# Kernel tuning notes

Hardware: AMD Instinct MI355X
Metric: run time of the kernel (lower is better)

The kernel has to match this reference:

```python
import jax, jax.numpy as jnp
import numpy as np

B, N, E, D = 32, 512, 2048, 128
N_STEPS = 3


def setup_inputs() -> dict:
    key = jax.random.key(0)
    ks = jax.random.split(key, 16)
    s = 0.05
    return {
        "prop_state": jax.random.normal(ks[0], (B, N, D), jnp.float32),
        "edge_states": jax.random.normal(ks[1], (B, E, D), jnp.float32),
        "A": jax.random.uniform(ks[2], (B, N, E), jnp.float32) / E,
        "tem_features": jax.random.normal(ks[3], (B, 64), jnp.float32),
        "link_W": jax.random.normal(ks[4], (D, D), jnp.float32) * s,
        "link_b": jnp.zeros((D,), jnp.float32),
        "reset_W": jax.random.normal(ks[5], (2 * D, D), jnp.float32) * s,
        "reset_b": jnp.zeros((D,), jnp.float32),
        "update_W": jax.random.normal(ks[6], (2 * D, D), jnp.float32) * s,
        "update_b": jnp.zeros((D,), jnp.float32),
        "trans_W": jax.random.normal(ks[7], (2 * D, D), jnp.float32) * s,
        "trans_b": jnp.zeros((D,), jnp.float32),
        "att_W1": jax.random.normal(ks[8], (D, D), jnp.float32) * s,
        "att_b1": jnp.zeros((D,), jnp.float32),
        "att_W2": jax.random.normal(ks[9], (D, 1), jnp.float32) * s,
        "att_b2": jnp.zeros((1,), jnp.float32),
        "out_W": jax.random.normal(ks[10], (D, D), jnp.float32) * s,
        "out_b": jnp.zeros((D,), jnp.float32),
    }


def reference(prop_state, edge_states, A, tem_features,
              link_W, link_b, reset_W, reset_b, update_W, update_b,
              trans_W, trans_b, att_W1, att_b1, att_W2, att_b2, out_W, out_b):
    init_node = prop_state
    init_edge = edge_states
    for _ in range(N_STEPS):
        edge_states = edge_states @ link_W + link_b              # [B,E,D]
        a_cur = jnp.einsum('bne,bed->bnd', A, edge_states)       # [B,N,D]
        a = jnp.concatenate([a_cur, prop_state], axis=2)         # [B,N,2D]
        r = jax.nn.sigmoid(a @ reset_W + reset_b)
        z = jax.nn.sigmoid(a @ update_W + update_b)
        joined = jnp.concatenate([a_cur, r * prop_state], axis=2)
        h_hat = jnp.tanh(joined @ trans_W + trans_b)
        prop_state = (1.0 - z) * prop_state + z * h_hat
    # attention pooling
    atten = jnp.tanh(prop_state @ att_W1 + att_b1) @ att_W2 + att_b2   # [B,N,1]
    Aw = jax.nn.softmax(jnp.transpose(atten, (0, 2, 1)), axis=2)       # [B,1,N]
    out = jnp.tanh(prop_state @ out_W + out_b)                         # [B,N,D]
    mul = jnp.einsum('bqn,bnd->bqd', Aw, out)                          # [B,1,D]
    graph_out = jnp.tanh(jnp.squeeze(mul, axis=1))                     # [B,D]
    # residual block: mean over concatenated node+edge initial states
    feat = jnp.concatenate([init_node, init_edge], axis=1)             # [B,N+E,D]
    residual = jnp.mean(feat, axis=1)                                  # [B,D]
    res = jax.nn.relu(graph_out + residual)
    return res, mul, edge_states
```

## Files before the change

### kernel.cpp

```cpp
#include <hip/hip_runtime.h>
#include <hip/hip_bf16.h>


typedef unsigned short u16;
typedef __attribute__((ext_vector_type(4))) float f32x4;
typedef __attribute__((ext_vector_type(8))) short bf16x8;

#define DI static __device__ __forceinline__

DI u16 f2bf(float f) {
    unsigned u = __builtin_bit_cast(unsigned, f);
    return (u16)((u + 0x7fffu + ((u >> 16) & 1u)) >> 16);
}
DI float bf2f(u16 h) { return __builtin_bit_cast(float, ((unsigned)h) << 16); }

DI bf16x8 cvt8(float4 a, float4 b) {
    u16 tmp[8] = {f2bf(a.x), f2bf(a.y), f2bf(a.z), f2bf(a.w),
                  f2bf(b.x), f2bf(b.y), f2bf(b.z), f2bf(b.w)};
    return *(const bf16x8*)tmp;
}

DI int imgIdx(int k, int n) {
    return (((k >> 5) * 128 + n) * 4 + (((k >> 3) & 3) ^ ((n >> 1) & 3))) * 8 + (k & 7);
}
DI bf16x8 wfragG(const u16* __restrict__ img, int kc, int tt, int l15, int quad) {
    return *(const bf16x8*)&img[(((kc * 128 + tt * 16 + l15) * 4) + (quad ^ ((l15 >> 1) & 3))) * 8];
}

#define MFMA16(a, b, c) __builtin_amdgcn_mfma_f32_16x16x32_bf16(a, b, c, 0, 0, 0)

__global__ __launch_bounds__(256) void k_prep1(
    const float* __restrict__ linkW, const float* __restrict__ resetW,
    const float* __restrict__ updateW, const float* __restrict__ transW,
    const float* __restrict__ attW1, const float* __restrict__ outW,
    float* __restrict__ W2, u16* __restrict__ linkImg, u16* __restrict__ WrImg,
    u16* __restrict__ WzImg, u16* __restrict__ WhImg, u16* __restrict__ attW1Img,
    u16* __restrict__ outWImg)
{
    int blk = blockIdx.x, t = threadIdx.x;
    if (blk < 64) {
        int idx = blk * 256 + t;
        int r = idx >> 7, c = idx & 127;
        float acc = 0.f;
        for (int k = 0; k < 128; k++) acc += linkW[r * 128 + k] * linkW[k * 128 + c];
        W2[r * 128 + c] = acc;
    } else {
        const float* src; u16* dst; int base;
        if (blk < 68)      { src = resetW;  dst = WrImg;    base = 64; }
        else if (blk < 72) { src = updateW; dst = WzImg;    base = 68; }
        else if (blk < 76) { src = transW;  dst = WhImg;    base = 72; }
        else if (blk < 78) { src = linkW;   dst = linkImg;  base = 76; }
        else if (blk < 80) { src = attW1;   dst = attW1Img; base = 78; }
        else               { src = outW;    dst = outWImg;  base = 80; }
        int off = (blk - base) * 8192;
        for (int i = 0; i < 32; i++) {
            int e = off + t + i * 256;
            int k = e >> 7, n = e & 127;
            dst[imgIdx(k, n)] = f2bf(src[e]);
        }
    }
}

__global__ __launch_bounds__(256) void k_prep2(
    const float* __restrict__ linkW, const float* __restrict__ linkb,
    const float* __restrict__ W2, u16* __restrict__ W3Img, float* __restrict__ ebias)
{
    int blk = blockIdx.x, t = threadIdx.x;
    if (blk < 64) {
        int idx = blk * 256 + t;
        int r = idx >> 7, c = idx & 127;
        float acc = 0.f;
        for (int k = 0; k < 128; k++) acc += W2[r * 128 + k] * linkW[k * 128 + c];
        W3Img[imgIdx(r, c)] = f2bf(acc);
    } else if (t < 128) {
        float acc = linkb[t];
        for (int k = 0; k < 128; k++) acc += linkb[k] * (W2[k * 128 + t] + linkW[k * 128 + t]);
        ebias[t] = acc;
    }
}

__global__ __launch_bounds__(256) void k_te(
    const float* __restrict__ E0, u16* __restrict__ Eswz, float* __restrict__ resid)
{
    __shared__ alignas(16) u16 sT[4096];
    __shared__ float sCol[128];
    int t = threadIdx.x, kc = blockIdx.x, b = blockIdx.y;
    const float* Eb = E0 + (size_t)b * 262144 + (size_t)kc * 32 * 128;
    if (t < 128) sCol[t] = 0.f;
    float part[4] = {0.f, 0.f, 0.f, 0.f};
    int ncol = (t & 31) * 4;
    for (int i = 0; i < 4; i++) {
        int f4i = t + i * 256;
        int k5 = f4i >> 5;
        float4 v = *(const float4*)&Eb[k5 * 128 + ncol];
        int g = k5 >> 3, o = k5 & 7;
        float vv[4] = {v.x, v.y, v.z, v.w};
#pragma unroll
        for (int j = 0; j < 4; j++) {
            int n = ncol + j;
            sT[(n * 4 + (g ^ ((n >> 1) & 3))) * 8 + o] = f2bf(vv[j]);
            part[j] += vv[j];
        }
    }
    __syncthreads();
#pragma unroll
    for (int j = 0; j < 4; j++) atomicAdd(&sCol[ncol + j], part[j]);
    u16* dst = Eswz + (size_t)b * 262144 + (size_t)kc * 4096;
    ((uint4*)dst)[t] = ((const uint4*)sT)[t];
    ((uint4*)dst)[t + 256] = ((const uint4*)sT)[t + 256];
    __syncthreads();
    if (t < 128) atomicAdd(&resid[b * 128 + t], sCol[t]);
}

__global__ __launch_bounds__(256, 3) void k_g0(
    const float* __restrict__ A, const u16* __restrict__ Eswz,
    u16* __restrict__ aOut, float* __restrict__ rowsum)
{
    __shared__ float sAcc[4][16][128];
    __shared__ float sRs[4][16];
    int t = threadIdx.x, wid = t >> 6, lane = t & 63, l15 = lane & 15, quad = lane >> 4;
    int bx = blockIdx.x;
    int g = bx >> 8, rmod = bx & 255;
    int b = (rmod & 7) + 8 * g;
    int s = (rmod >> 3) & 31;
    size_t r0 = (size_t)b * 512 + (size_t)s * 16;
    const u16* Eb = Eswz + (size_t)b * 262144;
    const float* Ar = A + (r0 + l15) * 2048;
    int kbase = wid * 16;

    f32x4 acc[8];
#pragma unroll
    for (int i = 0; i < 8; i++) acc[i] = (f32x4){0.f, 0.f, 0.f, 0.f};
    float rsum = 0.f;

    float4 xc = *(const float4*)&Ar[kbase * 32 + quad * 8];
    float4 yc = *(const float4*)&Ar[kbase * 32 + quad * 8 + 4];
    bf16x8 bc[8];
#pragma unroll
    for (int tt = 0; tt < 8; tt++) bc[tt] = wfragG(Eb, kbase, tt, l15, quad);

    for (int kc = 0; kc < 16; kc++) {
        int kg = kbase + kc;
        float4 xn, yn; bf16x8 bn[8];
        if (kc < 15) {
            xn = *(const float4*)&Ar[(kg + 1) * 32 + quad * 8];
            yn = *(const float4*)&Ar[(kg + 1) * 32 + quad * 8 + 4];
#pragma unroll
            for (int tt = 0; tt < 8; tt++) bn[tt] = wfragG(Eb, kg + 1, tt, l15, quad);
        }
        rsum += xc.x + xc.y + xc.z + xc.w + yc.x + yc.y + yc.z + yc.w;
        bf16x8 af = cvt8(xc, yc);
#pragma unroll
        for (int tt = 0; tt < 8; tt++) acc[tt] = MFMA16(af, bc[tt], acc[tt]);
        if (kc < 15) {
            xc = xn; yc = yn;
#pragma unroll
            for (int tt = 0; tt < 8; tt++) bc[tt] = bn[tt];
        }
    }
    rsum += __shfl_xor(rsum, 16);
    rsum += __shfl_xor(rsum, 32);
    if (quad == 0) sRs[wid][l15] = rsum;
#pragma unroll
    for (int tt = 0; tt < 8; tt++)
#pragma unroll
        for (int r = 0; r < 4; r++)
            sAcc[wid][quad * 4 + r][tt * 16 + l15] = acc[tt][r];
    __syncthreads();
    {
        int row = t >> 4, c8 = (t & 15) * 8;
        u16 o[8];
#pragma unroll
        for (int j = 0; j < 8; j++) {
            float v = sAcc[0][row][c8 + j] + sAcc[1][row][c8 + j] +
                      sAcc[2][row][c8 + j] + sAcc[3][row][c8 + j];
            o[j] = f2bf(v);
        }
        *(uint4*)&aOut[(r0 + row) * 128 + c8] = *(const uint4*)o;
    }
    if (t < 16)
        rowsum[r0 + t] = sRs[0][t] + sRs[1][t] + sRs[2][t] + sRs[3][t];
}

__global__ __launch_bounds__(64) void k_gates(
    u16* __restrict__ aBuf, const float* __restrict__ pIn, float* __restrict__ pOut,
    const float* __restrict__ rowsum,
    const u16* __restrict__ linkImg, const u16* __restrict__ WrImg,
    const u16* __restrict__ WzImg, const u16* __restrict__ WhImg,
    const float* __restrict__ link_b, const float* __restrict__ reset_b,
    const float* __restrict__ update_b, const float* __restrict__ trans_b)
{
    __shared__ alignas(16) u16 sT[16 * 136];
    int t = threadIdx.x, l15 = t & 15, quad = t >> 4;
    size_t r0 = (size_t)blockIdx.x * 16;

    bf16x8 aF[4], pF[4];
#pragma unroll
    for (int kc = 0; kc < 4; kc++) {
        aF[kc] = *(const bf16x8*)&aBuf[(r0 + l15) * 128 + kc * 32 + quad * 8];
        float4 x = *(const float4*)&pIn[(r0 + l15) * 128 + kc * 32 + quad * 8];
        float4 y = *(const float4*)&pIn[(r0 + l15) * 128 + kc * 32 + quad * 8 + 4];
        pF[kc] = cvt8(x, y);
    }

    f32x4 zero4 = {0.f, 0.f, 0.f, 0.f};
    f32x4 acc[8];
#pragma unroll
    for (int i = 0; i < 8; i++) acc[i] = zero4;
#pragma unroll
    for (int kc = 0; kc < 4; kc++)
#pragma unroll
        for (int tt = 0; tt < 8; tt++)
            acc[tt] = MFMA16(aF[kc], wfragG(linkImg, kc, tt, l15, quad), acc[tt]);
    float sv[4];
#pragma unroll
    for (int r = 0; r < 4; r++) sv[r] = rowsum[r0 + quad * 4 + r];
#pragma unroll
    for (int tt = 0; tt < 8; tt++) {
        int col = tt * 16 + l15; float lb = link_b[col];
#pragma unroll
        for (int r = 0; r < 4; r++)
            sT[(quad * 4 + r) * 136 + col] = f2bf(acc[tt][r] + sv[r] * lb);
    }
    __syncthreads();
#pragma unroll
    for (int kc = 0; kc < 4; kc++)
        aF[kc] = *(const bf16x8*)&sT[l15 * 136 + kc * 32 + quad * 8];
#pragma unroll
    for (int i = 0; i < 4; i++) {
        int idx = t + i * 64; int row = idx >> 4, col = (idx & 15) * 8;
        *(uint4*)&aBuf[(r0 + row) * 128 + col] = *(const uint4*)&sT[row * 136 + col];
    }

    f32x4 aR[8], aZ[8];
#pragma unroll
    for (int i = 0; i < 8; i++) { aR[i] = zero4; aZ[i] = zero4; }
#pragma unroll
    for (int kc = 0; kc < 8; kc++) {
        bf16x8 af = (kc < 4) ? aF[kc] : pF[kc - 4];
#pragma unroll
        for (int tt = 0; tt < 8; tt++) {
            aR[tt] = MFMA16(af, wfragG(WrImg, kc, tt, l15, quad), aR[tt]);
            aZ[tt] = MFMA16(af, wfragG(WzImg, kc, tt, l15, quad), aZ[tt]);
        }
    }
    __syncthreads();
#pragma unroll
    for (int tt = 0; tt < 8; tt++) {
        int col = tt * 16 + l15; float rb = reset_b[col], ub = update_b[col];
#pragma unroll
        for (int r = 0; r < 4; r++) {
            float rv = 1.f / (1.f + __expf(-(aR[tt][r] + rb)));
            aZ[tt][r] = 1.f / (1.f + __expf(-(aZ[tt][r] + ub)));
            float p = pIn[(r0 + quad * 4 + r) * 128 + col];
            sT[(quad * 4 + r) * 136 + col] = f2bf(rv * p);
        }
    }
    __syncthreads();
    bf16x8 rpF[4];
#pragma unroll
    for (int kc = 0; kc < 4; kc++)
        rpF[kc] = *(const bf16x8*)&sT[l15 * 136 + kc * 32 + quad * 8];

#pragma unroll
    for (int i = 0; i < 8; i++) aR[i] = zero4;
#pragma unroll
    for (int kc = 0; kc < 8; kc++) {
        bf16x8 af = (kc < 4) ? aF[kc] : rpF[kc - 4];
#pragma unroll
        for (int tt = 0; tt < 8; tt++)
            aR[tt] = MFMA16(af, wfragG(WhImg, kc, tt, l15, quad), aR[tt]);
    }
#pragma unroll
    for (int tt = 0; tt < 8; tt++) {
        int col = tt * 16 + l15; float tb = trans_b[col];
#pragma unroll
        for (int r = 0; r < 4; r++) {
            size_t row = r0 + quad * 4 + r;
            float h = tanhf(aR[tt][r] + tb);
            float z = aZ[tt][r];
            float p = pIn[row * 128 + col];
            pOut[row * 128 + col] = (1.f - z) * p + z * h;
        }
    }
}

__global__ __launch_bounds__(64) void k_att(
    const float* __restrict__ pIn, const u16* __restrict__ attW1Img,
    const u16* __restrict__ outWImg, const float* __restrict__ att_b1,
    const float* __restrict__ att_W2, const float* __restrict__ att_b2,
    const float* __restrict__ out_b, float* __restrict__ atten, float* __restrict__ outPool)
{
    int t = threadIdx.x, l15 = t & 15, quad = t >> 4;
    size_t r0 = (size_t)blockIdx.x * 16;
    bf16x8 pF[4];
#pragma unroll
    for (int kc = 0; kc < 4; kc++) {
        float4 x = *(const float4*)&pIn[(r0 + l15) * 128 + kc * 32 + quad * 8];
        float4 y = *(const float4*)&pIn[(r0 + l15) * 128 + kc * 32 + quad * 8 + 4];
        pF[kc] = cvt8(x, y);
    }
    f32x4 zero4 = {0.f, 0.f, 0.f, 0.f};
    f32x4 aA[8], aO[8];
#pragma unroll
    for (int i = 0; i < 8; i++) { aA[i] = zero4; aO[i] = zero4; }
#pragma unroll
    for (int kc = 0; kc < 4; kc++)
#pragma unroll
        for (int tt = 0; tt < 8; tt++) {
            aA[tt] = MFMA16(pF[kc], wfragG(attW1Img, kc, tt, l15, quad), aA[tt]);
            aO[tt] = MFMA16(pF[kc], wfragG(outWImg, kc, tt, l15, quad), aO[tt]);
        }
    float part[4] = {0.f, 0.f, 0.f, 0.f};
#pragma unroll
    for (int tt = 0; tt < 8; tt++) {
        int col = tt * 16 + l15;
        float b1 = att_b1[col], w2 = att_W2[col], ob = out_b[col];
#pragma unroll
        for (int r = 0; r < 4; r++) {
            part[r] += tanhf(aA[tt][r] + b1) * w2;
            outPool[(r0 + quad * 4 + r) * 128 + col] = tanhf(aO[tt][r] + ob);
        }
    }
    float b2 = att_b2[0];
#pragma unroll
    for (int r = 0; r < 4; r++) {
        float loc = part[r];
        loc += __shfl_xor(loc, 1); loc += __shfl_xor(loc, 2);
        loc += __shfl_xor(loc, 4); loc += __shfl_xor(loc, 8);
        if (l15 == 0) atten[r0 + quad * 4 + r] = loc + b2;
    }
}

__global__ __launch_bounds__(64) void k_eout(
    const float* __restrict__ E0, const u16* __restrict__ W3Img,
    const float* __restrict__ ebias, float* __restrict__ Eout)
{
    int t = threadIdx.x, l15 = t & 15, quad = t >> 4;
    size_t r0 = (size_t)blockIdx.x * 16;
    bf16x8 eF[4];
#pragma unroll
    for (int kc = 0; kc < 4; kc++) {
        float4 x = *(const float4*)&E0[(r0 + l15) * 128 + kc * 32 + quad * 8];
        float4 y = *(const float4*)&E0[(r0 + l15) * 128 + kc * 32 + quad * 8 + 4];
        eF[kc] = cvt8(x, y);
    }
    f32x4 zero4 = {0.f, 0.f, 0.f, 0.f};
    f32x4 acc[8];
#pragma unroll
    for (int i = 0; i < 8; i++) acc[i] = zero4;
#pragma unroll
    for (int kc = 0; kc < 4; kc++)
#pragma unroll
        for (int tt = 0; tt < 8; tt++)
            acc[tt] = MFMA16(eF[kc], wfragG(W3Img, kc, tt, l15, quad), acc[tt]);
#pragma unroll
    for (int tt = 0; tt < 8; tt++) {
        int col = tt * 16 + l15; float eb = ebias[col];
#pragma unroll
        for (int r = 0; r < 4; r++)
            Eout[(r0 + quad * 4 + r) * 128 + col] = acc[tt][r] + eb;
    }
}

__global__ __launch_bounds__(256) void k_fin(
    const float* __restrict__ atten, const float* __restrict__ outPool,
    const float* __restrict__ prop0, const float* __restrict__ resid,
    float* __restrict__ outRes, float* __restrict__ outMul)
{
    __shared__ float swv[512];
    __shared__ float sred[256];
    int t = threadIdx.x, b = blockIdx.x;
    float a0 = atten[b * 512 + t], a1 = atten[b * 512 + 256 + t];
    sred[t] = fmaxf(a0, a1); __syncthreads();
    for (int s = 128; s > 0; s >>= 1) { if (t < s) sred[t] = fmaxf(sred[t], sred[t + s]); __syncthreads(); }
    float mx = sred[0]; __syncthreads();
    float e0 = __expf(a0 - mx), e1 = __expf(a1 - mx);
    swv[t] = e0; swv[t + 256] = e1;
    sred[t] = e0 + e1; __syncthreads();
    for (int s = 128; s > 0; s >>= 1) { if (t < s) sred[t] += sred[t + s]; __syncthreads(); }
    float Z = sred[0]; __syncthreads();
    int col = t & 127, half = t >> 7;
    const float* op = outPool + ((size_t)b * 512 + half * 256) * 128 + col;
    const float* pp = prop0 + ((size_t)b * 512 + half * 256) * 128 + col;
    float accM = 0.f, accN = 0.f;
    for (int n = 0; n < 256; n++) {
        accM += swv[half * 256 + n] * op[(size_t)n * 128];
        accN += pp[(size_t)n * 128];
    }
    sred[t] = accM; __syncthreads();
    float mulv = 0.f;
    if (t < 128) mulv = (sred[t] + sred[t + 128]) / Z;
    __syncthreads();
    sred[t] = accN; __syncthreads();
    if (t < 128) {
        float nodesum = sred[t] + sred[t + 128];
        float rv = (nodesum + resid[b * 128 + t]) * (1.f / 2560.f);
        outMul[b * 128 + t] = mulv;
        outRes[b * 128 + t] = fmaxf(0.f, tanhf(mulv) + rv);
    }
}

extern "C" void kernel_launch(void* const* d_in, const int* in_sizes, int n_in,
                              void* d_out, int out_size, void* d_ws, size_t ws_size,
                              hipStream_t stream)
{
    const float* prop0  = (const float*)d_in[0];
    const float* edge0  = (const float*)d_in[1];
    const float* Amat   = (const float*)d_in[2];
    const float* linkW  = (const float*)d_in[4];
    const float* linkb  = (const float*)d_in[5];
    const float* resetW = (const float*)d_in[6];
    const float* resetb = (const float*)d_in[7];
    const float* updateW= (const float*)d_in[8];
    const float* updateb= (const float*)d_in[9];
    const float* transW = (const float*)d_in[10];
    const float* transb = (const float*)d_in[11];
    const float* attW1  = (const float*)d_in[12];
    const float* attb1  = (const float*)d_in[13];
    const float* attW2  = (const float*)d_in[14];
    const float* attb2  = (const float*)d_in[15];
    const float* outW   = (const float*)d_in[16];
    const float* outb   = (const float*)d_in[17];

    char* w = (char*)d_ws;
    u16*   ws_a_bf    = (u16*)(w);
    float* ws_prop    = (float*)(w + 4194304);
    float* ws_rowsum  = (float*)(w + 12582912);
    float* ws_atten   = (float*)(w + 12648448);
    float* ws_resid   = (float*)(w + 12713984);
    float* ws_W2      = (float*)(w + 12730368);
    float* ws_ebias   = (float*)(w + 12795904);
    u16*   ws_linkImg = (u16*)(w + 12796416);
    u16*   ws_W3Img   = (u16*)(w + 12829184);
    u16*   ws_WrImg   = (u16*)(w + 12861952);
    u16*   ws_WzImg   = (u16*)(w + 12927488);
    u16*   ws_WhImg   = (u16*)(w + 12993024);
    u16*   ws_attW1Img= (u16*)(w + 13058560);
    u16*   ws_outWImg = (u16*)(w + 13091328);

    float* out_res  = (float*)d_out;
    float* out_mul  = out_res + 4096;
    float* out_edge = out_res + 8192;
    u16*   Eswz     = (u16*)out_edge;
    float* outPool  = out_edge + 4194304;

    hipMemsetAsync(ws_resid, 0, 32 * 128 * sizeof(float), stream);
    k_prep1<<<82, 256, 0, stream>>>(linkW, resetW, updateW, transW, attW1, outW,
                                    ws_W2, ws_linkImg, ws_WrImg, ws_WzImg, ws_WhImg,
                                    ws_attW1Img, ws_outWImg);
    k_prep2<<<65, 256, 0, stream>>>(linkW, linkb, ws_W2, ws_W3Img, ws_ebias);
    k_te<<<dim3(64, 32), 256, 0, stream>>>(edge0, Eswz, ws_resid);
    k_g0<<<1024, 256, 0, stream>>>(Amat, Eswz, ws_a_bf, ws_rowsum);
    k_gates<<<1024, 64, 0, stream>>>(ws_a_bf, prop0, ws_prop, ws_rowsum,
                                     ws_linkImg, ws_WrImg, ws_WzImg, ws_WhImg,
                                     linkb, resetb, updateb, transb);
    k_gates<<<1024, 64, 0, stream>>>(ws_a_bf, ws_prop, ws_prop, ws_rowsum,
                                     ws_linkImg, ws_WrImg, ws_WzImg, ws_WhImg,
                                     linkb, resetb, updateb, transb);
    k_gates<<<1024, 64, 0, stream>>>(ws_a_bf, ws_prop, ws_prop, ws_rowsum,
                                     ws_linkImg, ws_WrImg, ws_WzImg, ws_WhImg,
                                     linkb, resetb, updateb, transb);
    k_att<<<1024, 64, 0, stream>>>(ws_prop, ws_attW1Img, ws_outWImg, attb1, attW2, attb2,
                                   outb, ws_atten, outPool);
    k_fin<<<32, 256, 0, stream>>>(ws_atten, outPool, prop0, ws_resid, out_res, out_mul);
    k_eout<<<4096, 64, 0, stream>>>(edge0, ws_W3Img, ws_ebias, out_edge);
}
```

Measured before the change: 396.3 us.

## Fuse attention into last gate step, prefetch weight fragments, parallelize prep and fin

The attention/output projection is folded into the third gate kernel, so the final propagation state no longer makes a round trip through global memory. The gate steps also store a bf16 copy of the state so the next step skips fp32 loads and conversion. Weight fragments are double-buffered in registers across k-chunks to hide load latency, and some __syncthreads are removed. The prep matmuls are split four ways with shuffle reductions, and k_fin uses 512 threads. The removed barriers sit on a shared sT buffer that different lanes read and write, which could be a race risk, and the prefetch buffers raise register pressure.

Measured after the change: 394.2 us. Within noise of the previous version (-0.5%).

```diff
diff --git a/kernel.cpp b/kernel.cpp
--- a/kernel.cpp
+++ b/kernel.cpp
@@ -38,20 +38,25 @@
     u16* __restrict__ outWImg)
 {
     int blk = blockIdx.x, t = threadIdx.x;
-    if (blk < 64) {
+    if (blk < 256) {
         int idx = blk * 256 + t;
-        int r = idx >> 7, c = idx & 127;
+        int out = idx >> 2, q = idx & 3;
+        int r = out >> 7, c = out & 127;
+        const float* ar = linkW + r * 128 + q * 32;
         float acc = 0.f;
-        for (int k = 0; k < 128; k++) acc += linkW[r * 128 + k] * linkW[k * 128 + c];
-        W2[r * 128 + c] = acc;
+#pragma unroll
+        for (int k = 0; k < 32; k++) acc += ar[k] * linkW[(q * 32 + k) * 128 + c];
+        acc += __shfl_xor(acc, 1);
+        acc += __shfl_xor(acc, 2);
+        if (q == 0) W2[out] = acc;
     } else {
         const float* src; u16* dst; int base;
-        if (blk < 68)      { src = resetW;  dst = WrImg;    base = 64; }
-        else if (blk < 72) { src = updateW; dst = WzImg;    base = 68; }
-        else if (blk < 76) { src = transW;  dst = WhImg;    base = 72; }
-        else if (blk < 78) { src = linkW;   dst = linkImg;  base = 76; }
-        else if (blk < 80) { src = attW1;   dst = attW1Img; base = 78; }
-        else               { src = outW;    dst = outWImg;  base = 80; }
+        if (blk < 260)      { src = resetW;  dst = WrImg;    base = 256; }
+        else if (blk < 264) { src = updateW; dst = WzImg;    base = 260; }
+        else if (blk < 268) { src = transW;  dst = WhImg;    base = 264; }
+        else if (blk < 270) { src = linkW;   dst = linkImg;  base = 268; }
+        else if (blk < 272) { src = attW1;   dst = attW1Img; base = 270; }
+        else                { src = outW;    dst = outWImg;  base = 272; }
         int off = (blk - base) * 8192;
         for (int i = 0; i < 32; i++) {
             int e = off + t + i * 256;
@@ -66,14 +71,20 @@
     const float* __restrict__ W2, u16* __restrict__ W3Img, float* __restrict__ ebias)
 {
     int blk = blockIdx.x, t = threadIdx.x;
-    if (blk < 64) {
+    if (blk < 256) {
         int idx = blk * 256 + t;
-        int r = idx >> 7, c = idx & 127;
+        int out = idx >> 2, q = idx & 3;
+        int r = out >> 7, c = out & 127;
+        const float* ar = W2 + r * 128 + q * 32;
         float acc = 0.f;
-        for (int k = 0; k < 128; k++) acc += W2[r * 128 + k] * linkW[k * 128 + c];
-        W3Img[imgIdx(r, c)] = f2bf(acc);
+#pragma unroll
+        for (int k = 0; k < 32; k++) acc += ar[k] * linkW[(q * 32 + k) * 128 + c];
+        acc += __shfl_xor(acc, 1);
+        acc += __shfl_xor(acc, 2);
+        if (q == 0) W3Img[imgIdx(r, c)] = f2bf(acc);
     } else if (t < 128) {
         float acc = linkb[t];
+#pragma unroll 8
         for (int k = 0; k < 128; k++) acc += linkb[k] * (W2[k * 128 + t] + linkW[k * 128 + t]);
         ebias[t] = acc;
     }
@@ -182,36 +193,61 @@
         rowsum[r0 + t] = sRs[0][t] + sRs[1][t] + sRs[2][t] + sRs[3][t];
 }
 
-__global__ __launch_bounds__(64) void k_gates(
+template<int DO_ATT>
+__global__ __launch_bounds__(64) void k_gates_t(
     u16* __restrict__ aBuf, const float* __restrict__ pIn, float* __restrict__ pOut,
+    u16* __restrict__ pBfOut, const u16* __restrict__ pBfIn, int first,
     const float* __restrict__ rowsum,
     const u16* __restrict__ linkImg, const u16* __restrict__ WrImg,
     const u16* __restrict__ WzImg, const u16* __restrict__ WhImg,
+    const u16* __restrict__ attW1Img, const u16* __restrict__ outWImg,
     const float* __restrict__ link_b, const float* __restrict__ reset_b,
-    const float* __restrict__ update_b, const float* __restrict__ trans_b)
+    const float* __restrict__ update_b, const float* __restrict__ trans_b,
+    const float* __restrict__ att_b1, const float* __restrict__ att_W2,
+    const float* __restrict__ att_b2, const float* __restrict__ out_b,
+    float* __restrict__ atten, float* __restrict__ outPool)
 {
     __shared__ alignas(16) u16 sT[16 * 136];
     int t = threadIdx.x, l15 = t & 15, quad = t >> 4;
     size_t r0 = (size_t)blockIdx.x * 16;
+    f32x4 zero4 = {0.f, 0.f, 0.f, 0.f};
 
     bf16x8 aF[4], pF[4];
 #pragma unroll
-    for (int kc = 0; kc < 4; kc++) {
+    for (int kc = 0; kc < 4; kc++)
         aF[kc] = *(const bf16x8*)&aBuf[(r0 + l15) * 128 + kc * 32 + quad * 8];
-        float4 x = *(const float4*)&pIn[(r0 + l15) * 128 + kc * 32 + quad * 8];
-        float4 y = *(const float4*)&pIn[(r0 + l15) * 128 + kc * 32 + quad * 8 + 4];
-        pF[kc] = cvt8(x, y);
-    }
-
-    f32x4 zero4 = {0.f, 0.f, 0.f, 0.f};
+    if (first) {
+#pragma unroll
+        for (int kc = 0; kc < 4; kc++) {
+            float4 x = *(const float4*)&pIn[(r0 + l15) * 128 + kc * 32 + quad * 8];
+            float4 y = *(const float4*)&pIn[(r0 + l15) * 128 + kc * 32 + quad * 8 + 4];
+            pF[kc] = cvt8(x, y);
+        }
+    } else {
+#pragma unroll
+        for (int kc = 0; kc < 4; kc++)
+            pF[kc] = *(const bf16x8*)&pBfIn[(r0 + l15) * 128 + kc * 32 + quad * 8];
+    }
+
     f32x4 acc[8];
 #pragma unroll
     for (int i = 0; i < 8; i++) acc[i] = zero4;
-#pragma unroll
-    for (int kc = 0; kc < 4; kc++)
-#pragma unroll
-        for (int tt = 0; tt < 8; tt++)
-            acc[tt] = MFMA16(aF[kc], wfragG(linkImg, kc, tt, l15, quad), acc[tt]);
+    {
+        bf16x8 wc[8], wn[8];
+#pragma unroll
+        for (int tt = 0; tt < 8; tt++) wc[tt] = wfragG(linkImg, 0, tt, l15, quad);
+#pragma unroll
+        for (int kc = 0; kc < 4; kc++) {
+            if (kc < 3)
+#pragma unroll
+                for (int tt = 0; tt < 8; tt++) wn[tt] = wfragG(linkImg, kc + 1, tt, l15, quad);
+#pragma unroll
+            for (int tt = 0; tt < 8; tt++) acc[tt] = MFMA16(aF[kc], wc[tt], acc[tt]);
+            if (kc < 3)
+#pragma unroll
+                for (int tt = 0; tt < 8; tt++) wc[tt] = wn[tt];
+        }
+    }
     float sv[4];
 #pragma unroll
     for (int r = 0; r < 4; r++) sv[r] = rowsum[r0 + quad * 4 + r];
@@ -222,29 +258,46 @@
         for (int r = 0; r < 4; r++)
             sT[(quad * 4 + r) * 136 + col] = f2bf(acc[tt][r] + sv[r] * lb);
     }
-    __syncthreads();
 #pragma unroll
     for (int kc = 0; kc < 4; kc++)
         aF[kc] = *(const bf16x8*)&sT[l15 * 136 + kc * 32 + quad * 8];
-#pragma unroll
-    for (int i = 0; i < 4; i++) {
-        int idx = t + i * 64; int row = idx >> 4, col = (idx & 15) * 8;
-        *(uint4*)&aBuf[(r0 + row) * 128 + col] = *(const uint4*)&sT[row * 136 + col];
+    if (!DO_ATT) {
+#pragma unroll
+        for (int i = 0; i < 4; i++) {
+            int idx = t + i * 64; int row = idx >> 4, col = (idx & 15) * 8;
+            *(uint4*)&aBuf[(r0 + row) * 128 + col] = *(const uint4*)&sT[row * 136 + col];
+        }
     }
 
     f32x4 aR[8], aZ[8];
 #pragma unroll
     for (int i = 0; i < 8; i++) { aR[i] = zero4; aZ[i] = zero4; }
-#pragma unroll
-    for (int kc = 0; kc < 8; kc++) {
-        bf16x8 af = (kc < 4) ? aF[kc] : pF[kc - 4];
+    {
+        bf16x8 rc[8], zc[8], rn[8], zn[8];
 #pragma unroll
         for (int tt = 0; tt < 8; tt++) {
-            aR[tt] = MFMA16(af, wfragG(WrImg, kc, tt, l15, quad), aR[tt]);
-            aZ[tt] = MFMA16(af, wfragG(WzImg, kc, tt, l15, quad), aZ[tt]);
-        }
-    }
-    __syncthreads();
+            rc[tt] = wfragG(WrImg, 0, tt, l15, quad);
+            zc[tt] = wfragG(WzImg, 0, tt, l15, quad);
+        }
+#pragma unroll
+        for (int kc = 0; kc < 8; kc++) {
+            if (kc < 7)
+#pragma unroll
+                for (int tt = 0; tt < 8; tt++) {
+                    rn[tt] = wfragG(WrImg, kc + 1, tt, l15, quad);
+                    zn[tt] = wfragG(WzImg, kc + 1, tt, l15, quad);
+                }
+            bf16x8 af = (kc < 4) ? aF[kc] : pF[kc - 4];
+#pragma unroll
+            for (int tt = 0; tt < 8; tt++) {
+                aR[tt] = MFMA16(af, rc[tt], aR[tt]);
+                aZ[tt] = MFMA16(af, zc[tt], aZ[tt]);
+            }
+            if (kc < 7)
+#pragma unroll
+                for (int tt = 0; tt < 8; tt++) { rc[tt] = rn[tt]; zc[tt] = zn[tt]; }
+        }
+    }
 #pragma unroll
     for (int tt = 0; tt < 8; tt++) {
         int col = tt * 16 + l15; float rb = reset_b[col], ub = update_b[col];
@@ -256,7 +309,6 @@
             sT[(quad * 4 + r) * 136 + col] = f2bf(rv * p);
         }
     }
-    __syncthreads();
     bf16x8 rpF[4];
 #pragma unroll
     for (int kc = 0; kc < 4; kc++)
@@ -264,12 +316,22 @@
 
 #pragma unroll
     for (int i = 0; i < 8; i++) aR[i] = zero4;
-#pragma unroll
-    for (int kc = 0; kc < 8; kc++) {
-        bf16x8 af = (kc < 4) ? aF[kc] : rpF[kc - 4];
-#pragma unroll
-        for (int tt = 0; tt < 8; tt++)
-            aR[tt] = MFMA16(af, wfragG(WhImg, kc, tt, l15, quad), aR[tt]);
+    {
+        bf16x8 wc[8], wn[8];
+#pragma unroll
+        for (int tt = 0; tt < 8; tt++) wc[tt] = wfragG(WhImg, 0, tt, l15, quad);
+#pragma unroll
+        for (int kc = 0; kc < 8; kc++) {
+            if (kc < 7)
+#pragma unroll
+                for (int tt = 0; tt < 8; tt++) wn[tt] = wfragG(WhImg, kc + 1, tt, l15, quad);
+            bf16x8 af = (kc < 4) ? aF[kc] : rpF[kc - 4];
+#pragma unroll
+            for (int tt = 0; tt < 8; tt++) aR[tt] = MFMA16(af, wc[tt], aR[tt]);
+            if (kc < 7)
+#pragma unroll
+                for (int tt = 0; tt < 8; tt++) wc[tt] = wn[tt];
+        }
     }
 #pragma unroll
     for (int tt = 0; tt < 8; tt++) {
@@ -280,37 +342,67 @@
             float h = tanhf(aR[tt][r] + tb);
             float z = aZ[tt][r];
             float p = pIn[row * 128 + col];
-            pOut[row * 128 + col] = (1.f - z) * p + z * h;
-        }
-    }
-}
-
-__global__ __launch_bounds__(64) void k_att(
-    const float* __restrict__ pIn, const u16* __restrict__ attW1Img,
-    const u16* __restrict__ outWImg, const float* __restrict__ att_b1,
-    const float* __restrict__ att_W2, const float* __restrict__ att_b2,
-    const float* __restrict__ out_b, float* __restrict__ atten, float* __restrict__ outPool)
-{
-    int t = threadIdx.x, l15 = t & 15, quad = t >> 4;
-    size_t r0 = (size_t)blockIdx.x * 16;
-    bf16x8 pF[4];
-#pragma unroll
-    for (int kc = 0; kc < 4; kc++) {
-        float4 x = *(const float4*)&pIn[(r0 + l15) * 128 + kc * 32 + quad * 8];
-        float4 y = *(const float4*)&pIn[(r0 + l15) * 128 + kc * 32 + quad * 8 + 4];
-        pF[kc] = cvt8(x, y);
-    }
-    f32x4 zero4 = {0.f, 0.f, 0.f, 0.f};
+            float pn = (1.f - z) * p + z * h;
+            acc[tt][r] = pn;
+            if (!DO_ATT) pOut[row * 128 + col] = pn;
+        }
+    }
+    if (!DO_ATT) {
+#pragma unroll
+        for (int tt = 0; tt < 8; tt++) {
+            int col = tt * 16 + l15;
+#pragma unroll
+            for (int r = 0; r < 4; r++)
+                sT[(quad * 4 + r) * 136 + col] = f2bf(acc[tt][r]);
+        }
+#pragma unroll
+        for (int i = 0; i < 4; i++) {
+            int idx = t + i * 64; int row = idx >> 4, col = (idx & 15) * 8;
+            *(uint4*)&pBfOut[(r0 + row) * 128 + col] = *(const uint4*)&sT[row * 136 + col];
+        }
+        return;
+    }
+
+#pragma unroll
+    for (int tt = 0; tt < 8; tt++) {
+        int col = tt * 16 + l15;
+#pragma unroll
+        for (int r = 0; r < 4; r++)
+            sT[(quad * 4 + r) * 136 + col] = f2bf(acc[tt][r]);
+    }
+    bf16x8 pnF[4];
+#pragma unroll
+    for (int kc = 0; kc < 4; kc++)
+        pnF[kc] = *(const bf16x8*)&sT[l15 * 136 + kc * 32 + quad * 8];
+
     f32x4 aA[8], aO[8];
 #pragma unroll
     for (int i = 0; i < 8; i++) { aA[i] = zero4; aO[i] = zero4; }
-#pragma unroll
-    for (int kc = 0; kc < 4; kc++)
+    {
+        bf16x8 ac[8], oc[8], an[8], on[8];
 #pragma unroll
         for (int tt = 0; tt < 8; tt++) {
-            aA[tt] = MFMA16(pF[kc], wfragG(attW1Img, kc, tt, l15, quad), aA[tt]);
-            aO[tt] = MFMA16(pF[kc], wfragG(outWImg, kc, tt, l15, quad), aO[tt]);
-        }
+            ac[tt] = wfragG(attW1Img, 0, tt, l15, quad);
+            oc[tt] = wfragG(outWImg, 0, tt, l15, quad);
+        }
+#pragma unroll
+        for (int kc = 0; kc < 4; kc++) {
+            if (kc < 3)
+#pragma unroll
+                for (int tt = 0; tt < 8; tt++) {
+                    an[tt] = wfragG(attW1Img, kc + 1, tt, l15, quad);
+                    on[tt] = wfragG(outWImg, kc + 1, tt, l15, quad);
+                }
+#pragma unroll
+            for (int tt = 0; tt < 8; tt++) {
+                aA[tt] = MFMA16(pnF[kc], ac[tt], aA[tt]);
+                aO[tt] = MFMA16(pnF[kc], oc[tt], aO[tt]);
+            }
+            if (kc < 3)
+#pragma unroll
+                for (int tt = 0; tt < 8; tt++) { ac[tt] = an[tt]; oc[tt] = on[tt]; }
+        }
+    }
     float part[4] = {0.f, 0.f, 0.f, 0.f};
 #pragma unroll
     for (int tt = 0; tt < 8; tt++) {
@@ -345,15 +437,25 @@
         float4 y = *(const float4*)&E0[(r0 + l15) * 128 + kc * 32 + quad * 8 + 4];
         eF[kc] = cvt8(x, y);
     }
-    f32x4 zero4 = {0.f, 0.f, 0.f, 0.f};
     f32x4 acc[8];
 #pragma unroll
-    for (int i = 0; i < 8; i++) acc[i] = zero4;
-#pragma unroll
-    for (int kc = 0; kc < 4; kc++)
-#pragma unroll
-        for (int tt = 0; tt < 8; tt++)
-            acc[tt] = MFMA16(eF[kc], wfragG(W3Img, kc, tt, l15, quad), acc[tt]);
+    for (int i = 0; i < 8; i++) acc[i] = (f32x4){0.f, 0.f, 0.f, 0.f};
+    {
+        bf16x8 wc[8], wn[8];
+#pragma unroll
+        for (int tt = 0; tt < 8; tt++) wc[tt] = wfragG(W3Img, 0, tt, l15, quad);
+#pragma unroll
+        for (int kc = 0; kc < 4; kc++) {
+            if (kc < 3)
+#pragma unroll
+                for (int tt = 0; tt < 8; tt++) wn[tt] = wfragG(W3Img, kc + 1, tt, l15, quad);
+#pragma unroll
+            for (int tt = 0; tt < 8; tt++) acc[tt] = MFMA16(eF[kc], wc[tt], acc[tt]);
+            if (kc < 3)
+#pragma unroll
+                for (int tt = 0; tt < 8; tt++) wc[tt] = wn[tt];
+        }
+    }
 #pragma unroll
     for (int tt = 0; tt < 8; tt++) {
         int col = tt * 16 + l15; float eb = ebias[col];
@@ -363,38 +465,36 @@
     }
 }
 
-__global__ __launch_bounds__(256) void k_fin(
+__global__ __launch_bounds__(512) void k_fin(
     const float* __restrict__ atten, const float* __restrict__ outPool,
     const float* __restrict__ prop0, const float* __restrict__ resid,
     float* __restrict__ outRes, float* __restrict__ outMul)
 {
     __shared__ float swv[512];
-    __shared__ float sred[256];
+    __shared__ float sred[512];
+    __shared__ float sacc[8][128];
     int t = threadIdx.x, b = blockIdx.x;
-    float a0 = atten[b * 512 + t], a1 = atten[b * 512 + 256 + t];
-    sred[t] = fmaxf(a0, a1); __syncthreads();
-    for (int s = 128; s > 0; s >>= 1) { if (t < s) sred[t] = fmaxf(sred[t], sred[t + s]); __syncthreads(); }
+    float a = atten[b * 512 + t];
+    sred[t] = a; __syncthreads();
+    for (int s = 256; s > 0; s >>= 1) { if (t < s) sred[t] = fmaxf(sred[t], sred[t + s]); __syncthreads(); }
     float mx = sred[0]; __syncthreads();
-    float e0 = __expf(a0 - mx), e1 = __expf(a1 - mx);
-    swv[t] = e0; swv[t + 256] = e1;
-    sred[t] = e0 + e1; __syncthreads();
-    for (int s = 128; s > 0; s >>= 1) { if (t < s) sred[t] += sred[t + s]; __syncthreads(); }
+    float e = __expf(a - mx);
+    swv[t] = e; sred[t] = e; __syncthreads();
+    for (int s = 256; s > 0; s >>= 1) { if (t < s) sred[t] += sred[t + s]; __syncthreads(); }
     float Z = sred[0]; __syncthreads();
-    int col = t & 127, half = t >> 7;
-    const float* op = outPool + ((size_t)b * 512 + half * 256) * 128 + col;
-    const float* pp = prop0 + ((size_t)b * 512 + half * 256) * 128 + col;
+    int col = t & 127, q = t >> 7;
+    const float* op = outPool + ((size_t)b * 512 + q * 128) * 128 + col;
+    const float* pp = prop0 + ((size_t)b * 512 + q * 128) * 128 + col;
     float accM = 0.f, accN = 0.f;
-    for (int n = 0; n < 256; n++) {
-        accM += swv[half * 256 + n] * op[(size_t)n * 128];
+    for (int n = 0; n < 128; n++) {
+        accM += swv[q * 128 + n] * op[(size_t)n * 128];
         accN += pp[(size_t)n * 128];
     }
-    sred[t] = accM; __syncthreads();
-    float mulv = 0.f;
-    if (t < 128) mulv = (sred[t] + sred[t + 128]) / Z;
+    sacc[q][col] = accM; sacc[4 + q][col] = accN;
     __syncthreads();
-    sred[t] = accN; __syncthreads();
     if (t < 128) {
-        float nodesum = sred[t] + sred[t + 128];
+        float mulv = (sacc[0][t] + sacc[1][t] + sacc[2][t] + sacc[3][t]) / Z;
+        float nodesum = sacc[4][t] + sacc[5][t] + sacc[6][t] + sacc[7][t];
         float rv = (nodesum + resid[b * 128 + t]) * (1.f / 2560.f);
         outMul[b * 128 + t] = mulv;
         outRes[b * 128 + t] = fmaxf(0.f, tanhf(mulv) + rv);
@@ -426,18 +526,19 @@
     char* w = (char*)d_ws;
     u16*   ws_a_bf    = (u16*)(w);
     float* ws_prop    = (float*)(w + 4194304);
-    float* ws_rowsum  = (float*)(w + 12582912);
-    float* ws_atten   = (float*)(w + 12648448);
-    float* ws_resid   = (float*)(w + 12713984);
-    float* ws_W2      = (float*)(w + 12730368);
-    float* ws_ebias   = (float*)(w + 12795904);
-    u16*   ws_linkImg = (u16*)(w + 12796416);
-    u16*   ws_W3Img   = (u16*)(w + 12829184);
-    u16*   ws_WrImg   = (u16*)(w + 12861952);
-    u16*   ws_WzImg   = (u16*)(w + 12927488);
-    u16*   ws_WhImg   = (u16*)(w + 12993024);
-    u16*   ws_attW1Img= (u16*)(w + 13058560);
-    u16*   ws_outWImg = (u16*)(w + 13091328);
+    u16*   ws_prop_bf = (u16*)(w + 12582912);
+    float* ws_rowsum  = (float*)(w + 16777216);
+    float* ws_atten   = (float*)(w + 16842752);
+    float* ws_resid   = (float*)(w + 16908288);
+    float* ws_W2      = (float*)(w + 16924672);
+    float* ws_ebias   = (float*)(w + 16990208);
+    u16*   ws_linkImg = (u16*)(w + 16990720);
+    u16*   ws_W3Img   = (u16*)(w + 17023488);
+    u16*   ws_WrImg   = (u16*)(w + 17056256);
+    u16*   ws_WzImg   = (u16*)(w + 17121792);
+    u16*   ws_WhImg   = (u16*)(w + 17187328);
+    u16*   ws_attW1Img= (u16*)(w + 17252864);
+    u16*   ws_outWImg = (u16*)(w + 17285632);
 
     float* out_res  = (float*)d_out;
     float* out_mul  = out_res + 4096;
@@ -446,23 +547,27 @@
     float* outPool  = out_edge + 4194304;
 
     hipMemsetAsync(ws_resid, 0, 32 * 128 * sizeof(float), stream);
-    k_prep1<<<82, 256, 0, stream>>>(linkW, resetW, updateW, transW, attW1, outW,
-                                    ws_W2, ws_linkImg, ws_WrImg, ws_WzImg, ws_WhImg,
-                                    ws_attW1Img, ws_outWImg);
-    k_prep2<<<65, 256, 0, stream>>>(linkW, linkb, ws_W2, ws_W3Img, ws_ebias);
+    k_prep1<<<274, 256, 0, stream>>>(linkW, resetW, updateW, transW, attW1, outW,
+                                     ws_W2, ws_linkImg, ws_WrImg, ws_WzImg, ws_WhImg,
+                                     ws_attW1Img, ws_outWImg);
+    k_prep2<<<257, 256, 0, stream>>>(linkW, linkb, ws_W2, ws_W3Img, ws_ebias);
     k_te<<<dim3(64, 32), 256, 0, stream>>>(edge0, Eswz, ws_resid);
     k_g0<<<1024, 256, 0, stream>>>(Amat, Eswz, ws_a_bf, ws_rowsum);
-    k_gates<<<1024, 64, 0, stream>>>(ws_a_bf, prop0, ws_prop, ws_rowsum,
-                                     ws_linkImg, ws_WrImg, ws_WzImg, ws_WhImg,
-                                     linkb, resetb, updateb, transb);
-    k_gates<<<1024, 64, 0, stream>>>(ws_a_bf, ws_prop, ws_prop, ws_rowsum,
-                                     ws_linkImg, ws_WrImg, ws_WzImg, ws_WhImg,
-                                     linkb, resetb, updateb, transb);
-    k_gates<<<1024, 64, 0, stream>>>(ws_a_bf, ws_prop, ws_prop, ws_rowsum,
-                                     ws_linkImg, ws_WrImg, ws_WzImg, ws_WhImg,
-                                     linkb, resetb, updateb, transb);
-    k_att<<<1024, 64, 0, stream>>>(ws_prop, ws_attW1Img, ws_outWImg, attb1, attW2, attb2,
-                                   outb, ws_atten, outPool);
-    k_fin<<<32, 256, 0, stream>>>(ws_atten, outPool, prop0, ws_resid, out_res, out_mul);
+    k_gates_t<0><<<1024, 64, 0, stream>>>(ws_a_bf, prop0, ws_prop, ws_prop_bf, ws_prop_bf, 1,
+                                          ws_rowsum, ws_linkImg, ws_WrImg, ws_WzImg, ws_WhImg,
+                                          ws_attW1Img, ws_outWImg,
+                                          linkb, resetb, updateb, transb,
+                                          attb1, attW2, attb2, outb, ws_atten, outPool);
+    k_gates_t<0><<<1024, 64, 0, stream>>>(ws_a_bf, ws_prop, ws_prop, ws_prop_bf, ws_prop_bf, 0,
+                                          ws_rowsum, ws_linkImg, ws_WrImg, ws_WzImg, ws_WhImg,
+                                          ws_attW1Img, ws_outWImg,
+                                          linkb, resetb, updateb, transb,
+                                          attb1, attW2, attb2, outb, ws_atten, outPool);
+    k_gates_t<1><<<1024, 64, 0, stream>>>(ws_a_bf, ws_prop, ws_prop, ws_prop_bf, ws_prop_bf, 0,
+                                          ws_rowsum, ws_linkImg, ws_WrImg, ws_WzImg, ws_WhImg,
+                                          ws_attW1Img, ws_outWImg,
+                                          linkb, resetb, updateb, transb,
+                                          attb1, attW2, attb2, outb, ws_atten, outPool);
+    k_fin<<<32, 512, 0, stream>>>(ws_atten, outPool, prop0, ws_resid, out_res, out_mul);
     k_eout<<<4096, 64, 0, stream>>>(edge0, ws_W3Img, ws_ebias, out_edge);
 }
```
